# Optimization experiments

Measured on AMD Instinct MI355X. Metric: run time of the kernel, lower is better.

Reference implementation:

```python
import jax, jax.numpy as jnp
import numpy as np

N_NODES = 50000
N_EDGES = 400000
N_GRAPHS = 32
EMB = 64
EDGE_DIM = 4
IN_DIM = 11
LAYERS = 4
EPS = 1e-5


def _bn(x, g, b):
    # BatchNorm1d in train mode: biased batch statistics over rows
    m = jnp.mean(x, axis=0)
    v = jnp.mean(jnp.square(x - m), axis=0)
    return g * (x - m) * jax.lax.rsqrt(v + EPS) + b


def setup_inputs() -> dict:
    key = jax.random.key(0)
    ks = jax.random.split(key, 16)
    x = jax.random.normal(ks[0], (N_NODES, IN_DIM), dtype=jnp.float32)
    edge_attr = jax.random.normal(ks[1], (N_EDGES, EDGE_DIM), dtype=jnp.float32)
    edge_index = jax.random.randint(ks[2], (2, N_EDGES), 0, N_NODES, dtype=jnp.int32)
    batch = jnp.sort(jax.random.randint(ks[3], (N_NODES,), 0, N_GRAPHS, dtype=jnp.int32))

    def lin(k, fan_in, shape):
        bound = 1.0 / np.sqrt(fan_in)
        return jax.random.uniform(k, shape, jnp.float32, -bound, bound)

    msg_in = 2 * EMB + EDGE_DIM  # 132
    upd_in = 2 * EMB             # 128
    kk = jax.random.split(ks[4], 12)
    params = dict(
        lin_in_W=lin(kk[0], IN_DIM, (IN_DIM, EMB)),
        lin_in_b=lin(kk[1], IN_DIM, (EMB,)),
        msg_W1=lin(kk[2], msg_in, (LAYERS, msg_in, EMB)),
        msg_b1=lin(kk[3], msg_in, (LAYERS, EMB)),
        msg_g1=jnp.ones((LAYERS, EMB), jnp.float32),
        msg_be1=jnp.zeros((LAYERS, EMB), jnp.float32),
        msg_W2=lin(kk[4], EMB, (LAYERS, EMB, EMB)),
        msg_b2=lin(kk[5], EMB, (LAYERS, EMB)),
        msg_g2=jnp.ones((LAYERS, EMB), jnp.float32),
        msg_be2=jnp.zeros((LAYERS, EMB), jnp.float32),
        upd_W1=lin(kk[6], upd_in, (LAYERS, upd_in, EMB)),
        upd_b1=lin(kk[7], upd_in, (LAYERS, EMB)),
        upd_g1=jnp.ones((LAYERS, EMB), jnp.float32),
        upd_be1=jnp.zeros((LAYERS, EMB), jnp.float32),
        upd_W2=lin(kk[8], EMB, (LAYERS, EMB, EMB)),
        upd_b2=lin(kk[9], EMB, (LAYERS, EMB)),
        upd_g2=jnp.ones((LAYERS, EMB), jnp.float32),
        upd_be2=jnp.zeros((LAYERS, EMB), jnp.float32),
        pred_W=lin(kk[10], EMB, (EMB, 1)),
        pred_b=lin(kk[11], EMB, (1,)),
    )
    return dict(x=x, edge_attr=edge_attr, edge_index=edge_index, batch=batch, **params)


def reference(x, edge_attr, edge_index, batch, lin_in_W, lin_in_b,
              msg_W1, msg_b1, msg_g1, msg_be1, msg_W2, msg_b2, msg_g2, msg_be2,
              upd_W1, upd_b1, upd_g1, upd_be1, upd_W2, upd_b2, upd_g2, upd_be2,
              pred_W, pred_b):
    src = edge_index[0]  # j (source)
    dst = edge_index[1]  # i (target, PyG default flow source_to_target)
    h = x @ lin_in_W + lin_in_b  # (n, d)
    for l in range(LAYERS):
        m_in = jnp.concatenate([h[dst], h[src], edge_attr], axis=-1)  # (e, 2d+d_e)
        m = jax.nn.relu(_bn(m_in @ msg_W1[l] + msg_b1[l], msg_g1[l], msg_be1[l]))
        m = jax.nn.relu(_bn(m @ msg_W2[l] + msg_b2[l], msg_g2[l], msg_be2[l]))
        aggr = jax.ops.segment_sum(m, dst, num_segments=N_NODES)  # scatter-add
        u_in = jnp.concatenate([h, aggr], axis=-1)  # (n, 2d)
        u = jax.nn.relu(_bn(u_in @ upd_W1[l] + upd_b1[l], upd_g1[l], upd_be1[l]))
        u = jax.nn.relu(_bn(u @ upd_W2[l] + upd_b2[l], upd_g2[l], upd_be2[l]))
        h = h + u  # residual in MPNNModel.forward
    sums = jax.ops.segment_sum(h, batch, num_segments=N_GRAPHS)
    counts = jax.ops.segment_sum(jnp.ones((h.shape[0],), h.dtype), batch, num_segments=N_GRAPHS)
    h_graph = sums / jnp.maximum(counts, 1.0)[:, None]  # global_mean_pool
    out = h_graph @ pred_W + pred_b  # (G, 1)
    return out.reshape(-1)
```

## Files before the change

kernel.cpp:

```cpp
#include <hip/hip_runtime.h>

#define DEV __device__ __forceinline__

constexpr int NN = 50000;
constexpr int NE = 400000;
constexpr int NG = 32;
constexpr float EPSV = 1e-5f;
constexpr int SCAN_BLOCKS = 196;
constexpr int NSHARD = 8;
constexpr int STB = NSHARD * 128;

constexpr int ECB = 2048;
constexpr int ESLOT = ECB * 256 / 8;

typedef __attribute__((ext_vector_type(8))) short s16x8;
typedef __attribute__((ext_vector_type(4))) float f32x4;

DEV unsigned short f2b(float f) {
  union { float f; unsigned u; } x; x.f = f;
  unsigned r = x.u + 0x7fffu + ((x.u >> 16) & 1u);
  return (unsigned short)(r >> 16);
}
DEV float b2f(unsigned short u) {
  union { unsigned u; float f; } x; x.u = ((unsigned)u) << 16; return x.f;
}

DEV s16x8 frag_from_f32(const float* p) {
  const float4 v0 = *(const float4*)p;
  const float4 v1 = *(const float4*)(p + 4);
  s16x8 af;
  af[0] = (short)f2b(v0.x); af[1] = (short)f2b(v0.y);
  af[2] = (short)f2b(v0.z); af[3] = (short)f2b(v0.w);
  af[4] = (short)f2b(v1.x); af[5] = (short)f2b(v1.y);
  af[6] = (short)f2b(v1.z); af[7] = (short)f2b(v1.w);
  return af;
}

DEV void ld8(float* d, const float* p) {
  float4 a = *(const float4*)p;
  float4 b = *(const float4*)(p + 4);
  d[0] = a.x; d[1] = a.y; d[2] = a.z; d[3] = a.w;
  d[4] = b.x; d[5] = b.y; d[6] = b.z; d[7] = b.w;
}

DEV void bn_coeff(const float* __restrict__ st, const float* __restrict__ g,
                  const float* __restrict__ be, float invM, int c,
                  float& sc, float& sh) {
  float s = 0.f, s2 = 0.f;
#pragma unroll
  for (int k = 0; k < NSHARD; ++k) {
    s += st[k * 128 + c];
    s2 += st[k * 128 + 64 + c];
  }
  float mean = s * invM;
  float var = s2 * invM - mean * mean;
  sc = g[c] * rsqrtf(var + EPSV);
  sh = be[c] - mean * sc;
}

__global__ __launch_bounds__(256) void lin_in_kernel(
    const float* __restrict__ x, const float* __restrict__ W,
    const float* __restrict__ b, float* __restrict__ h)
{
  int gid = blockIdx.x * 256 + threadIdx.x;
  if (gid >= NN * 64) return;
  int n = gid >> 6, c = gid & 63;
  float acc = b[c];
#pragma unroll
  for (int k = 0; k < 11; ++k)
    acc = fmaf(x[n * 11 + k], W[k * 64 + c], acc);
  h[gid] = acc;
}

__global__ __launch_bounds__(256) void hist_kernel(
    const int* __restrict__ dstI, int* __restrict__ deg)
{
  int e = blockIdx.x * 256 + threadIdx.x;
  if (e < NE) atomicAdd(&deg[dstI[e]], 1);
}

__global__ __launch_bounds__(256) void scan_pass1(
    const int* __restrict__ deg, int* __restrict__ blockSums)
{
  __shared__ int red[4];
  int tid = threadIdx.x;
  int idx = blockIdx.x * 256 + tid;
  int v = (idx < NN) ? deg[idx] : 0;
#pragma unroll
  for (int off = 32; off > 0; off >>= 1) v += __shfl_down(v, off, 64);
  if ((tid & 63) == 0) red[tid >> 6] = v;
  __syncthreads();
  if (tid == 0) blockSums[blockIdx.x] = red[0] + red[1] + red[2] + red[3];
}

__global__ __launch_bounds__(256) void scan_pass2(
    const int* __restrict__ blockSums, int* __restrict__ blockOffs)
{
  __shared__ int part[256];
  int tid = threadIdx.x;
  int v = (tid < SCAN_BLOCKS) ? blockSums[tid] : 0;
  part[tid] = v;
  __syncthreads();
  for (int off = 1; off < 256; off <<= 1) {
    int t = 0;
    if (tid >= off) t = part[tid - off];
    __syncthreads();
    if (tid >= off) part[tid] += t;
    __syncthreads();
  }
  blockOffs[tid] = (tid == 0) ? 0 : part[tid - 1];
}

__global__ __launch_bounds__(256) void scan_pass3(
    const int* __restrict__ deg, const int* __restrict__ blockOffs,
    int* __restrict__ rowptr, int* __restrict__ cursor)
{
  __shared__ int part[256];
  int tid = threadIdx.x;
  int idx = blockIdx.x * 256 + tid;
  int v = (idx < NN) ? deg[idx] : 0;
  part[tid] = v;
  __syncthreads();
  for (int off = 1; off < 256; off <<= 1) {
    int t = 0;
    if (tid >= off) t = part[tid - off];
    __syncthreads();
    if (tid >= off) part[tid] += t;
    __syncthreads();
  }
  int excl = (tid == 0) ? 0 : part[tid - 1];
  int val = blockOffs[blockIdx.x] + excl;
  if (idx < NN) { rowptr[idx] = val; cursor[idx] = val; }
  if (idx == 0) rowptr[NN] = NE;
}

__global__ __launch_bounds__(256) void fill_pos_kernel(
    const int* __restrict__ dstI, int* __restrict__ cursor,
    int* __restrict__ eid)
{
  int e = blockIdx.x * 256 + threadIdx.x;
  if (e < NE) {
    int pos = atomicAdd(&cursor[dstI[e]], 1);
    eid[pos] = e;
  }
}

__global__ __launch_bounds__(256) void permute_kernel(
    const int* __restrict__ eid, const int* __restrict__ srcI,
    const int* __restrict__ dstI, const float* __restrict__ ea,
    int* __restrict__ srcP, int* __restrict__ dstP,
    float* __restrict__ eaP)
{
  int p = blockIdx.x * 256 + threadIdx.x;
  if (p < NE) {
    int e = eid[p];
    srcP[p] = srcI[e];
    dstP[p] = dstI[e];
    *(float4*)&eaP[(size_t)p * 4] = *(const float4*)&ea[(size_t)e * 4];
  }
}

__global__ __launch_bounds__(256) void gemm_dual_mfma(
    float* __restrict__ h, const float* __restrict__ W,
    const unsigned short* __restrict__ u2,
    const float* __restrict__ st, const float* __restrict__ g,
    const float* __restrict__ be, float invM,
    unsigned short* __restrict__ Hd, unsigned short* __restrict__ Hs)
{
  __shared__ __align__(16) unsigned short Wt_s[2 * 64 * 72];
  __shared__ float sc_s[64], sh_s[64];

  const int tid = threadIdx.x;
  const int lane = tid & 63;
  const int wave = tid >> 6;
  const int nn = lane & 15;
  const int kq = lane >> 4;

  if (u2 != nullptr && tid < 64) {
    float sc, sh;
    bn_coeff(st, g, be, invM, tid, sc, sh);
    sc_s[tid] = sc;
    sh_s[tid] = sh;
  }
#pragma unroll
  for (int i = 0; i < 32; ++i) {
    int idx = i * 256 + tid;
    int half = idx >> 12;
    int rem = idx & 4095;
    int k = rem >> 6, n = rem & 63;
    Wt_s[half * 4608 + n * 72 + k] = f2b(W[idx]);
  }
  __syncthreads();

  s16x8 bfrag[2][4][2];
#pragma unroll
  for (int o = 0; o < 2; ++o)
#pragma unroll
    for (int nt = 0; nt < 4; ++nt)
#pragma unroll
      for (int kc = 0; kc < 2; ++kc) {
        const unsigned short* p =
            &Wt_s[o * 4608 + (nt * 16 + nn) * 72 + kc * 32 + kq * 8];
#pragma unroll
        for (int j = 0; j < 8; ++j) bfrag[o][nt][kc][j] = (short)p[j];
      }

  const int rbase = blockIdx.x * 128 + wave * 32;

  f32x4 acc[2][2][4];
#pragma unroll
  for (int o = 0; o < 2; ++o)
#pragma unroll
    for (int rt = 0; rt < 2; ++rt)
#pragma unroll
      for (int nt = 0; nt < 4; ++nt) acc[o][rt][nt] = (f32x4){0.f, 0.f, 0.f, 0.f};

#pragma unroll
  for (int rt = 0; rt < 2; ++rt) {
    int row = rbase + rt * 16 + nn;
    int rowc = row < NN ? row : NN - 1;
#pragma unroll
    for (int kc = 0; kc < 2; ++kc) {
      const int c0k = kc * 32 + kq * 8;
      s16x8 af;
      if (u2 != nullptr) {
        float* hp = &h[(size_t)rowc * 64 + c0k];
        float hv[8];
        ld8(hv, hp);
        uint4 uv = *(const uint4*)&u2[(size_t)rowc * 64 + c0k];
        const unsigned uw[4] = {uv.x, uv.y, uv.z, uv.w};
#pragma unroll
        for (int d = 0; d < 4; ++d) {
          union { unsigned u; float f; } lo, hi;
          lo.u = (uw[d] & 0xffffu) << 16;
          hi.u = uw[d] & 0xffff0000u;
          int j0 = d * 2, j1 = d * 2 + 1;
          hv[j0] += fmaxf(fmaf(sc_s[c0k + j0], lo.f, sh_s[c0k + j0]), 0.f);
          hv[j1] += fmaxf(fmaf(sc_s[c0k + j1], hi.f, sh_s[c0k + j1]), 0.f);
        }
        if (row < NN) {
          *(float4*)hp = make_float4(hv[0], hv[1], hv[2], hv[3]);
          *(float4*)(hp + 4) = make_float4(hv[4], hv[5], hv[6], hv[7]);
        }
#pragma unroll
        for (int j = 0; j < 8; ++j) af[j] = (short)f2b(hv[j]);
      } else {
        af = frag_from_f32(&h[(size_t)rowc * 64 + c0k]);
      }
#pragma unroll
      for (int o = 0; o < 2; ++o)
#pragma unroll
        for (int nt = 0; nt < 4; ++nt)
          acc[o][rt][nt] = __builtin_amdgcn_mfma_f32_16x16x32_bf16(
              af, bfrag[o][nt][kc], acc[o][rt][nt], 0, 0, 0);
    }
  }

#pragma unroll
  for (int rt = 0; rt < 2; ++rt)
#pragma unroll
    for (int nt = 0; nt < 4; ++nt) {
      int col = nt * 16 + nn;
#pragma unroll
      for (int reg = 0; reg < 4; ++reg) {
        int row = rbase + rt * 16 + kq * 4 + reg;
        if (row < NN) {
          Hd[(size_t)row * 64 + col] = f2b(acc[0][rt][nt][reg]);
          Hs[(size_t)row * 64 + col] = f2b(acc[1][rt][nt][reg]);
        }
      }
    }
}

__global__ __launch_bounds__(256) void edge_combine(
    const unsigned short* __restrict__ Hd, const unsigned short* __restrict__ Hs,
    const float* __restrict__ eaP, const int* __restrict__ srcP,
    const int* __restrict__ dstP, const float* __restrict__ Wb,
    const float* __restrict__ bias, unsigned short* __restrict__ t1,
    float* __restrict__ outStats)
{
  __shared__ float red_s[128];
  const int tid = threadIdx.x;
  const int c0 = (tid & 7) * 8;
  float bv[8], w0[8], w1[8], w2[8], w3[8];
#pragma unroll
  for (int j = 0; j < 8; ++j) {
    bv[j] = bias[c0 + j];
    w0[j] = Wb[0 * 64 + c0 + j];
    w1[j] = Wb[1 * 64 + c0 + j];
    w2[j] = Wb[2 * 64 + c0 + j];
    w3[j] = Wb[3 * 64 + c0 + j];
  }

  float s[8], s2[8];
#pragma unroll
  for (int j = 0; j < 8; ++j) { s[j] = 0.f; s2[j] = 0.f; }

  const int e0 = (blockIdx.x * 256 + tid) >> 3;

  int eiA[4];
  float4 avA[4];
  uint4 hdA[4], hsA[4];
#pragma unroll
  for (int u = 0; u < 4; ++u) {
    int ec = e0 + u * ESLOT;
    eiA[u] = ec;
    int si = srcP[ec], di = dstP[ec];
    avA[u] = *(const float4*)&eaP[(size_t)ec * 4];
    hdA[u] = *(const uint4*)&Hd[(size_t)di * 64 + c0];
    hsA[u] = *(const uint4*)&Hs[(size_t)si * 64 + c0];
  }

  int eiB[3];
  bool hasB[3];
  float4 avB[3];
  uint4 hdB[3], hsB[3];
#pragma unroll
  for (int u = 0; u < 3; ++u) {
    int ee = e0 + (4 + u) * ESLOT;
    hasB[u] = ee < NE;
    int ec = hasB[u] ? ee : e0;
    eiB[u] = ec;
    int si = srcP[ec], di = dstP[ec];
    avB[u] = *(const float4*)&eaP[(size_t)ec * 4];
    hdB[u] = *(const uint4*)&Hd[(size_t)di * 64 + c0];
    hsB[u] = *(const uint4*)&Hs[(size_t)si * 64 + c0];
  }

#pragma unroll
  for (int u = 0; u < 4; ++u) {
    const unsigned hdw[4] = {hdA[u].x, hdA[u].y, hdA[u].z, hdA[u].w};
    const unsigned hsw[4] = {hsA[u].x, hsA[u].y, hsA[u].z, hsA[u].w};
    const float4 av = avA[u];
    unsigned short ob[8];
#pragma unroll
    for (int d = 0; d < 4; ++d) {
      union { unsigned uu; float f; } a0, a1, b0, b1u;
      a0.uu = (hdw[d] & 0xffffu) << 16; a1.uu = hdw[d] & 0xffff0000u;
      b0.uu = (hsw[d] & 0xffffu) << 16; b1u.uu = hsw[d] & 0xffff0000u;
      int j0 = d * 2, j1 = d * 2 + 1;
      float y0 = a0.f + b0.f + bv[j0] + av.x * w0[j0] + av.y * w1[j0] + av.z * w2[j0] + av.w * w3[j0];
      float y1 = a1.f + b1u.f + bv[j1] + av.x * w0[j1] + av.y * w1[j1] + av.z * w2[j1] + av.w * w3[j1];
      ob[j0] = f2b(y0); ob[j1] = f2b(y1);
      s[j0] += y0; s2[j0] += y0 * y0;
      s[j1] += y1; s2[j1] += y1 * y1;
    }
    *(uint4*)&t1[(size_t)eiA[u] * 64 + c0] = *(const uint4*)ob;
  }

#pragma unroll
  for (int u = 0; u < 3; ++u) {
    if (!hasB[u]) continue;
    const unsigned hdw[4] = {hdB[u].x, hdB[u].y, hdB[u].z, hdB[u].w};
    const unsigned hsw[4] = {hsB[u].x, hsB[u].y, hsB[u].z, hsB[u].w};
    const float4 av = avB[u];
    unsigned short ob[8];
#pragma unroll
    for (int d = 0; d < 4; ++d) {
      union { unsigned uu; float f; } a0, a1, b0, b1u;
      a0.uu = (hdw[d] & 0xffffu) << 16; a1.uu = hdw[d] & 0xffff0000u;
      b0.uu = (hsw[d] & 0xffffu) << 16; b1u.uu = hsw[d] & 0xffff0000u;
      int j0 = d * 2, j1 = d * 2 + 1;
      float y0 = a0.f + b0.f + bv[j0] + av.x * w0[j0] + av.y * w1[j0] + av.z * w2[j0] + av.w * w3[j0];
      float y1 = a1.f + b1u.f + bv[j1] + av.x * w0[j1] + av.y * w1[j1] + av.z * w2[j1] + av.w * w3[j1];
      ob[j0] = f2b(y0); ob[j1] = f2b(y1);
      s[j0] += y0; s2[j0] += y0 * y0;
      s[j1] += y1; s2[j1] += y1 * y1;
    }
    *(uint4*)&t1[(size_t)eiB[u] * 64 + c0] = *(const uint4*)ob;
  }

#pragma unroll
  for (int j = 0; j < 8; ++j) {
    s[j] += __shfl_xor(s[j], 8, 64);
    s[j] += __shfl_xor(s[j], 16, 64);
    s[j] += __shfl_xor(s[j], 32, 64);
    s2[j] += __shfl_xor(s2[j], 8, 64);
    s2[j] += __shfl_xor(s2[j], 16, 64);
    s2[j] += __shfl_xor(s2[j], 32, 64);
  }
  if (tid < 128) red_s[tid] = 0.f;
  __syncthreads();
  if ((tid & 63) < 8) {
#pragma unroll
    for (int j = 0; j < 8; ++j) {
      atomicAdd(&red_s[c0 + j], s[j]);
      atomicAdd(&red_s[64 + c0 + j], s2[j]);
    }
  }
  __syncthreads();
  if (tid < 128)
    atomicAdd(&outStats[(blockIdx.x & (NSHARD - 1)) * 128 + tid], red_s[tid]);
}

__global__ __launch_bounds__(256) void gemm64_bn_mfma(
    const unsigned short* A0,
    const float* __restrict__ W,
    const float* __restrict__ bias,
    const float* __restrict__ inStats,
    const float* __restrict__ inG,
    const float* __restrict__ inBe,
    float invM_in,
    unsigned short* outp,
    float* __restrict__ outStats,
    int M)
{
  __shared__ __align__(16) unsigned short Wt_s[64 * 72];
  __shared__ float scale_s[64];
  __shared__ float shift_s[64];
  __shared__ float red_s[128];

  const int tid = threadIdx.x;
  const int lane = tid & 63;
  const int wave = tid >> 6;
  const int nn = lane & 15;
  const int kq = lane >> 4;

  if (tid < 64) {
    float sc, sh;
    bn_coeff(inStats, inG, inBe, invM_in, tid, sc, sh);
    scale_s[tid] = sc;
    shift_s[tid] = sh;
  }
#pragma unroll
  for (int i = 0; i < 16; ++i) {
    int idx = i * 256 + tid;
    int k = idx >> 6, n = idx & 63;
    Wt_s[n * 72 + k] = f2b(W[idx]);
  }
  __syncthreads();

  s16x8 bfrag[4][2];
#pragma unroll
  for (int nt = 0; nt < 4; ++nt)
#pragma unroll
    for (int kc = 0; kc < 2; ++kc)
      bfrag[nt][kc] = *(const s16x8*)&Wt_s[(nt * 16 + nn) * 72 + kc * 32 + kq * 8];

  float scf[2][8], shf[2][8];
#pragma unroll
  for (int kc = 0; kc < 2; ++kc) {
    int k0 = kc * 32 + kq * 8;
    ld8(scf[kc], &scale_s[k0]);
    ld8(shf[kc], &shift_s[k0]);
  }

  float bcol[4];
#pragma unroll
  for (int nt = 0; nt < 4; ++nt) bcol[nt] = bias[nt * 16 + nn];

  float s[4] = {0.f, 0.f, 0.f, 0.f};
  float s2[4] = {0.f, 0.f, 0.f, 0.f};

  uint4 raw[4][2];
  f32x4 acc[4][4];

  const int rb0 = blockIdx.x * 512 + wave * 64;
#pragma unroll
  for (int rt = 0; rt < 4; ++rt) {
    int row = rb0 + rt * 16 + nn;
    int rowc = row < M ? row : M - 1;
#pragma unroll
    for (int kc = 0; kc < 2; ++kc)
      raw[rt][kc] = *(const uint4*)&A0[(size_t)rowc * 64 + kc * 32 + kq * 8];
  }

#pragma unroll
  for (int rt = 0; rt < 4; ++rt)
#pragma unroll
    for (int nt = 0; nt < 4; ++nt) acc[rt][nt] = (f32x4){0.f, 0.f, 0.f, 0.f};
#pragma unroll
  for (int rt = 0; rt < 4; ++rt) {
#pragma unroll
    for (int kc = 0; kc < 2; ++kc) {
      unsigned wbits[4] = {raw[rt][kc].x, raw[rt][kc].y, raw[rt][kc].z, raw[rt][kc].w};
      s16x8 af;
#pragma unroll
      for (int d = 0; d < 4; ++d) {
        union { unsigned u; float f; } lo, hi;
        lo.u = (wbits[d] & 0xffffu) << 16;
        hi.u = wbits[d] & 0xffff0000u;
        int j0 = d * 2, j1 = d * 2 + 1;
        af[j0] = (short)f2b(fmaxf(fmaf(scf[kc][j0], lo.f, shf[kc][j0]), 0.f));
        af[j1] = (short)f2b(fmaxf(fmaf(scf[kc][j1], hi.f, shf[kc][j1]), 0.f));
      }
#pragma unroll
      for (int nt = 0; nt < 4; ++nt)
        acc[rt][nt] = __builtin_amdgcn_mfma_f32_16x16x32_bf16(
            af, bfrag[nt][kc], acc[rt][nt], 0, 0, 0);
    }
  }

  const int rb1 = rb0 + 256;
#pragma unroll
  for (int rt = 0; rt < 4; ++rt) {
    int row = rb1 + rt * 16 + nn;
    int rowc = row < M ? row : M - 1;
#pragma unroll
    for (int kc = 0; kc < 2; ++kc)
      raw[rt][kc] = *(const uint4*)&A0[(size_t)rowc * 64 + kc * 32 + kq * 8];
  }

#pragma unroll
  for (int rt = 0; rt < 4; ++rt)
#pragma unroll
    for (int nt = 0; nt < 4; ++nt) {
      int col = nt * 16 + nn;
#pragma unroll
      for (int reg = 0; reg < 4; ++reg) {
        int row = rb0 + rt * 16 + kq * 4 + reg;
        if (row < M) {
          float y = acc[rt][nt][reg] + bcol[nt];
          outp[(size_t)row * 64 + col] = f2b(y);
          s[nt] += y; s2[nt] += y * y;
        }
      }
    }

#pragma unroll
  for (int rt = 0; rt < 4; ++rt)
#pragma unroll
    for (int nt = 0; nt < 4; ++nt) acc[rt][nt] = (f32x4){0.f, 0.f, 0.f, 0.f};
#pragma unroll
  for (int rt = 0; rt < 4; ++rt) {
#pragma unroll
    for (int kc = 0; kc < 2; ++kc) {
      unsigned wbits[4] = {raw[rt][kc].x, raw[rt][kc].y, raw[rt][kc].z, raw[rt][kc].w};
      s16x8 af;
#pragma unroll
      for (int d = 0; d < 4; ++d) {
        union { unsigned u; float f; } lo, hi;
        lo.u = (wbits[d] & 0xffffu) << 16;
        hi.u = wbits[d] & 0xffff0000u;
        int j0 = d * 2, j1 = d * 2 + 1;
        af[j0] = (short)f2b(fmaxf(fmaf(scf[kc][j0], lo.f, shf[kc][j0]), 0.f));
        af[j1] = (short)f2b(fmaxf(fmaf(scf[kc][j1], hi.f, shf[kc][j1]), 0.f));
      }
#pragma unroll
      for (int nt = 0; nt < 4; ++nt)
        acc[rt][nt] = __builtin_amdgcn_mfma_f32_16x16x32_bf16(
            af, bfrag[nt][kc], acc[rt][nt], 0, 0, 0);
    }
  }

#pragma unroll
  for (int rt = 0; rt < 4; ++rt)
#pragma unroll
    for (int nt = 0; nt < 4; ++nt) {
      int col = nt * 16 + nn;
#pragma unroll
      for (int reg = 0; reg < 4; ++reg) {
        int row = rb1 + rt * 16 + kq * 4 + reg;
        if (row < M) {
          float y = acc[rt][nt][reg] + bcol[nt];
          outp[(size_t)row * 64 + col] = f2b(y);
          s[nt] += y; s2[nt] += y * y;
        }
      }
    }

#pragma unroll
  for (int nt = 0; nt < 4; ++nt) {
    s[nt] += __shfl_xor(s[nt], 16, 64);
    s[nt] += __shfl_xor(s[nt], 32, 64);
    s2[nt] += __shfl_xor(s2[nt], 16, 64);
    s2[nt] += __shfl_xor(s2[nt], 32, 64);
  }
  if (tid < 128) red_s[tid] = 0.f;
  __syncthreads();
  if (lane < 16) {
#pragma unroll
    for (int nt = 0; nt < 4; ++nt) {
      atomicAdd(&red_s[nt * 16 + nn], s[nt]);
      atomicAdd(&red_s[64 + nt * 16 + nn], s2[nt]);
    }
  }
  __syncthreads();
  if (tid < 128)
    atomicAdd(&outStats[(blockIdx.x & (NSHARD - 1)) * 128 + tid], red_s[tid]);
}

__global__ __launch_bounds__(256) void gemm_concat_mfma(
    const float* __restrict__ A0,
    const unsigned short* __restrict__ A1b,
    const float* __restrict__ W,
    const float* __restrict__ bias,
    unsigned short* __restrict__ outp,
    float* __restrict__ outStats,
    int M)
{
  __shared__ __align__(16) unsigned short Wt_s[64 * 136];
  __shared__ float red_s[128];

  const int tid = threadIdx.x;
  const int lane = tid & 63;
  const int wave = tid >> 6;
  const int nn = lane & 15;
  const int kq = lane >> 4;

#pragma unroll
  for (int i = 0; i < 32; ++i) {
    int idx = i * 256 + tid;
    int k = idx >> 6, n = idx & 63;
    Wt_s[n * 136 + k] = f2b(W[idx]);
  }
  __syncthreads();

  s16x8 bfrag[4][4];
#pragma unroll
  for (int nt = 0; nt < 4; ++nt)
#pragma unroll
    for (int kc = 0; kc < 4; ++kc) {
      const unsigned short* p = &Wt_s[(nt * 16 + nn) * 136 + kc * 32 + kq * 8];
#pragma unroll
      for (int j = 0; j < 8; ++j) bfrag[nt][kc][j] = (short)p[j];
    }

  const int rbase = blockIdx.x * 128 + wave * 32;

  f32x4 acc[2][4];
#pragma unroll
  for (int rt = 0; rt < 2; ++rt)
#pragma unroll
    for (int nt = 0; nt < 4; ++nt) acc[rt][nt] = (f32x4){0.f, 0.f, 0.f, 0.f};

#pragma unroll
  for (int rt = 0; rt < 2; ++rt) {
    int row = rbase + rt * 16 + nn;
    int rowc = row < M ? row : M - 1;
#pragma unroll
    for (int kc = 0; kc < 4; ++kc) {
      s16x8 af;
      if (kc < 2) {
        af = frag_from_f32(&A0[(size_t)rowc * 64 + kc * 32 + kq * 8]);
      } else {
        af = *(const s16x8*)&A1b[(size_t)rowc * 64 + (kc - 2) * 32 + kq * 8];
      }
#pragma unroll
      for (int nt = 0; nt < 4; ++nt)
        acc[rt][nt] = __builtin_amdgcn_mfma_f32_16x16x32_bf16(
            af, bfrag[nt][kc], acc[rt][nt], 0, 0, 0);
    }
  }

  float bcol[4];
#pragma unroll
  for (int nt = 0; nt < 4; ++nt) bcol[nt] = bias[nt * 16 + nn];

  float s[4] = {0.f, 0.f, 0.f, 0.f};
  float s2[4] = {0.f, 0.f, 0.f, 0.f};
#pragma unroll
  for (int rt = 0; rt < 2; ++rt)
#pragma unroll
    for (int nt = 0; nt < 4; ++nt) {
      int col = nt * 16 + nn;
#pragma unroll
      for (int reg = 0; reg < 4; ++reg) {
        int row = rbase + rt * 16 + kq * 4 + reg;
        if (row < M) {
          float y = acc[rt][nt][reg] + bcol[nt];
          outp[(size_t)row * 64 + col] = f2b(y);
          s[nt] += y; s2[nt] += y * y;
        }
      }
    }
#pragma unroll
  for (int nt = 0; nt < 4; ++nt) {
    s[nt] += __shfl_xor(s[nt], 16, 64);
    s[nt] += __shfl_xor(s[nt], 32, 64);
    s2[nt] += __shfl_xor(s2[nt], 16, 64);
    s2[nt] += __shfl_xor(s2[nt], 32, 64);
  }
  if (tid < 128) red_s[tid] = 0.f;
  __syncthreads();
  if (lane < 16) {
#pragma unroll
    for (int nt = 0; nt < 4; ++nt) {
      atomicAdd(&red_s[nt * 16 + nn], s[nt]);
      atomicAdd(&red_s[64 + nt * 16 + nn], s2[nt]);
    }
  }
  __syncthreads();
  if (tid < 128)
    atomicAdd(&outStats[(blockIdx.x & (NSHARD - 1)) * 128 + tid], red_s[tid]);
}

__global__ __launch_bounds__(256) void aggregate_kernel(
    const unsigned short* __restrict__ t2, const int* __restrict__ rowptr,
    const float* __restrict__ stats, const float* __restrict__ g,
    const float* __restrict__ be, float invM,
    unsigned short* __restrict__ aggr)
{
  __shared__ float sc_s[64], sh_s[64];
  const int tid = threadIdx.x;
  if (tid < 64) {
    float sc, sh;
    bn_coeff(stats, g, be, invM, tid, sc, sh);
    sc_s[tid] = sc;
    sh_s[tid] = sh;
  }
  __syncthreads();

  int node = (blockIdx.x * 256 + tid) >> 6;
  int lane = tid & 63;
  if (node >= NN) return;
  const int c8 = (lane & 7) * 8;
  const int rq = lane >> 3;

  float sc[8], sh[8];
#pragma unroll
  for (int j = 0; j < 8; ++j) {
    sc[j] = sc_s[c8 + j];
    sh[j] = sh_s[c8 + j];
  }

  int lo = rowptr[node], hi = rowptr[node + 1];
  float acc[8] = {0.f, 0.f, 0.f, 0.f, 0.f, 0.f, 0.f, 0.f};

  for (int i = lo; i < hi; i += 16) {
    int r0 = i + rq;
    int r1 = i + 8 + rq;
    bool h0 = r0 < hi, h1 = r1 < hi;
    uint4 v0 = make_uint4(0u, 0u, 0u, 0u), v1 = make_uint4(0u, 0u, 0u, 0u);
    if (h0) v0 = *(const uint4*)&t2[(size_t)r0 * 64 + c8];
    if (h1) v1 = *(const uint4*)&t2[(size_t)r1 * 64 + c8];
    if (h0) {
      const unsigned w[4] = {v0.x, v0.y, v0.z, v0.w};
#pragma unroll
      for (int d = 0; d < 4; ++d) {
        union { unsigned u; float f; } a0, a1;
        a0.u = (w[d] & 0xffffu) << 16;
        a1.u = w[d] & 0xffff0000u;
        acc[d * 2] += fmaxf(fmaf(sc[d * 2], a0.f, sh[d * 2]), 0.f);
        acc[d * 2 + 1] += fmaxf(fmaf(sc[d * 2 + 1], a1.f, sh[d * 2 + 1]), 0.f);
      }
    }
    if (h1) {
      const unsigned w[4] = {v1.x, v1.y, v1.z, v1.w};
#pragma unroll
      for (int d = 0; d < 4; ++d) {
        union { unsigned u; float f; } a0, a1;
        a0.u = (w[d] & 0xffffu) << 16;
        a1.u = w[d] & 0xffff0000u;
        acc[d * 2] += fmaxf(fmaf(sc[d * 2], a0.f, sh[d * 2]), 0.f);
        acc[d * 2 + 1] += fmaxf(fmaf(sc[d * 2 + 1], a1.f, sh[d * 2 + 1]), 0.f);
      }
    }
  }
#pragma unroll
  for (int j = 0; j < 8; ++j) {
    acc[j] += __shfl_xor(acc[j], 8, 64);
    acc[j] += __shfl_xor(acc[j], 16, 64);
    acc[j] += __shfl_xor(acc[j], 32, 64);
  }
  if (rq == 0) {
    unsigned short o[8];
#pragma unroll
    for (int j = 0; j < 8; ++j) o[j] = f2b(acc[j]);
    *(uint4*)&aggr[(size_t)node * 64 + c8] = *(const uint4*)o;
  }
}

constexpr int POOL_NPB = 128;

__global__ __launch_bounds__(256) void pool_partial(
    const float* __restrict__ h, const unsigned short* __restrict__ u2,
    const float* __restrict__ st, const float* __restrict__ g,
    const float* __restrict__ be, float invM,
    const int* __restrict__ batch, float* __restrict__ sums)
{
  int lane = threadIdx.x & 63;
  int wave = threadIdx.x >> 6;
  float sc, sh;
  bn_coeff(st, g, be, invM, lane, sc, sh);
  int base = blockIdx.x * POOL_NPB;
  float acc = 0.f;
  int gcur = -1;
  for (int i = wave; i < POOL_NPB; i += 4) {
    int n = base + i;
    if (n >= NN) break;
    int gb = batch[n];
    if (gb != gcur) {
      if (gcur >= 0) atomicAdd(&sums[gcur * 64 + lane], acc);
      gcur = gb;
      acc = 0.f;
    }
    acc += h[(size_t)n * 64 + lane] +
           fmaxf(fmaf(sc, b2f(u2[(size_t)n * 64 + lane]), sh), 0.f);
  }
  if (gcur >= 0) atomicAdd(&sums[gcur * 64 + lane], acc);
}

DEV int lower_bound_i(const int* __restrict__ a, int n, int v) {
  int lo = 0, hi = n;
  while (lo < hi) {
    int m = (lo + hi) >> 1;
    if (a[m] < v) lo = m + 1; else hi = m;
  }
  return lo;
}

__global__ __launch_bounds__(64) void pool_final(
    const float* __restrict__ sums, const int* __restrict__ batch,
    const float* __restrict__ predW, const float* __restrict__ predB,
    float* __restrict__ out)
{
  int g = blockIdx.x;
  int lane = threadIdx.x;
  int lo = lower_bound_i(batch, NN, g);
  int hi = lower_bound_i(batch, NN, g + 1);
  float cnt = fmaxf((float)(hi - lo), 1.0f);
  float p = sums[g * 64 + lane] / cnt * predW[lane];
#pragma unroll
  for (int off = 32; off > 0; off >>= 1) p += __shfl_down(p, off, 64);
  if (lane == 0) out[g] = p + predB[0];
}

extern "C" void kernel_launch(void* const* d_in, const int* in_sizes, int n_in,
                              void* d_out, int out_size, void* d_ws, size_t ws_size,
                              hipStream_t stream)
{
  (void)in_sizes; (void)n_in; (void)out_size; (void)ws_size;

  const float* x        = (const float*)d_in[0];
  const float* edge_attr= (const float*)d_in[1];
  const int*   eidx     = (const int*)d_in[2];
  const int*   batch    = (const int*)d_in[3];
  const float* linW     = (const float*)d_in[4];
  const float* linB     = (const float*)d_in[5];
  const float* msgW1    = (const float*)d_in[6];
  const float* msgB1    = (const float*)d_in[7];
  const float* msgG1    = (const float*)d_in[8];
  const float* msgBe1   = (const float*)d_in[9];
  const float* msgW2    = (const float*)d_in[10];
  const float* msgB2    = (const float*)d_in[11];
  const float* msgG2    = (const float*)d_in[12];
  const float* msgBe2   = (const float*)d_in[13];
  const float* updW1    = (const float*)d_in[14];
  const float* updB1    = (const float*)d_in[15];
  const float* updG1    = (const float*)d_in[16];
  const float* updBe1   = (const float*)d_in[17];
  const float* updW2    = (const float*)d_in[18];
  const float* updB2    = (const float*)d_in[19];
  const float* updG2    = (const float*)d_in[20];
  const float* updBe2   = (const float*)d_in[21];
  const float* predW    = (const float*)d_in[22];
  const float* predB    = (const float*)d_in[23];

  const int* srcI = eidx;
  const int* dstI = eidx + NE;

  char* p = (char*)d_ws;
  float* h  = (float*)p;            p += (size_t)NN * 64 * 4;
  unsigned short* t1 = (unsigned short*)p; p += (size_t)NE * 64 * 2;
  unsigned short* aggr = (unsigned short*)p; p += (size_t)NN * 64 * 2;
  unsigned short* u1 = (unsigned short*)p;   p += (size_t)NN * 64 * 2;
  unsigned short* Hd = (unsigned short*)p;   p += (size_t)NN * 64 * 2;
  unsigned short* Hs = (unsigned short*)p;   p += (size_t)NN * 64 * 2;
  float* stats = (float*)p;         p += 16 * STB * 4;
  float* sums = (float*)p;          p += NG * 64 * 4;
  int* deg = (int*)p;               p += (size_t)NN * 4;
  int* cursor = (int*)p;            p += (size_t)NN * 4;
  int* rowptr = (int*)p;            p += (size_t)(NN + 1) * 4;
  int* eid = (int*)p;               p += (size_t)NE * 4;
  int* srcP = (int*)p;              p += (size_t)NE * 4;
  int* dstP = (int*)p;              p += (size_t)NE * 4;
  float* eaP = (float*)p;           p += (size_t)NE * 4 * 4;
  int* blockSums = (int*)p;         p += 256 * 4;
  int* blockOffs = (int*)p;         p += 256 * 4;

  hipMemsetAsync(stats, 0, (size_t)(16 * STB + NG * 64 + NN) * 4, stream);

  hist_kernel<<<(NE + 255) / 256, 256, 0, stream>>>(dstI, deg);
  scan_pass1<<<SCAN_BLOCKS, 256, 0, stream>>>(deg, blockSums);
  scan_pass2<<<1, 256, 0, stream>>>(blockSums, blockOffs);
  scan_pass3<<<SCAN_BLOCKS, 256, 0, stream>>>(deg, blockOffs, rowptr, cursor);
  fill_pos_kernel<<<(NE + 255) / 256, 256, 0, stream>>>(dstI, cursor, eid);
  permute_kernel<<<(NE + 255) / 256, 256, 0, stream>>>(
      eid, srcI, dstI, edge_attr, srcP, dstP, eaP);

  lin_in_kernel<<<(NN * 64 + 255) / 256, 256, 0, stream>>>(x, linW, linB, h);

  const float invE = 1.0f / (float)NE;
  const float invN = 1.0f / (float)NN;
  const int NB128 = (NN + 127) / 128;
  const int NB512 = (NN + 511) / 512;
  const int EB512 = (NE + 511) / 512;

  for (int l = 0; l < 4; ++l) {
    float* st0 = stats + (l * 4 + 0) * STB;
    float* st1 = stats + (l * 4 + 1) * STB;
    float* st2 = stats + (l * 4 + 2) * STB;
    float* st3 = stats + (l * 4 + 3) * STB;
    const float* W1 = msgW1 + (size_t)l * 132 * 64;

    const unsigned short* prevU2 = (l == 0) ? nullptr : u1;
    const float* pst = (l == 0) ? stats : stats + ((l - 1) * 4 + 3) * STB;
    const float* pg  = (l == 0) ? updG2 : updG2 + (l - 1) * 64;
    const float* pbe = (l == 0) ? updBe2 : updBe2 + (l - 1) * 64;

    gemm_dual_mfma<<<NB128, 256, 0, stream>>>(
        h, W1, prevU2, pst, pg, pbe, invN, Hd, Hs);

    edge_combine<<<ECB, 256, 0, stream>>>(
        Hd, Hs, eaP, srcP, dstP, W1 + 128 * 64, msgB1 + l * 64,
        t1, st0);

    gemm64_bn_mfma<<<EB512, 256, 0, stream>>>(
        t1, msgW2 + (size_t)l * 64 * 64, msgB2 + l * 64,
        st0, msgG1 + l * 64, msgBe1 + l * 64, invE,
        t1, st1, NE);

    aggregate_kernel<<<(NN * 64 + 255) / 256, 256, 0, stream>>>(
        t1, rowptr, st1, msgG2 + l * 64, msgBe2 + l * 64, invE, aggr);

    gemm_concat_mfma<<<NB128, 256, 0, stream>>>(
        h, aggr, updW1 + (size_t)l * 128 * 64, updB1 + l * 64,
        u1, st2, NN);

    gemm64_bn_mfma<<<NB512, 256, 0, stream>>>(
        u1, updW2 + (size_t)l * 64 * 64, updB2 + l * 64,
        st2, updG1 + l * 64, updBe1 + l * 64, invN,
        u1, st3, NN);
  }

  pool_partial<<<(NN + POOL_NPB - 1) / POOL_NPB, 256, 0, stream>>>(
      h, u1, stats + (3 * 4 + 3) * STB, updG2 + 3 * 64, updBe2 + 3 * 64, invN,
      batch, sums);
  pool_final<<<NG, 64, 0, stream>>>(sums, batch, predW, predB, (float*)d_out);
}
```

Baseline: 630.5 us.

## Fuse CSR aggregation into update GEMM and merge setup kernels

The segment-sum aggregation (BN+ReLU applied on the fly) now runs inside the update-MLP first GEMM kernel. Each block aggregates 32 nodes into shared memory and then runs the MFMA GEMM with each wave owning a 16-column slice. This removes the aggr buffer round trip and one launch per layer, at the cost of a smaller block tile and weights reloaded from global memory per block. The histogram is also merged with the input linear layer, the scan's middle pass is folded into the last pass, and pool_partial computes BN coefficients once per block into shared memory.

```diff
diff --git a/kernel.cpp b/kernel.cpp
--- a/kernel.cpp
+++ b/kernel.cpp
@@ -58,25 +58,21 @@
   sh = be[c] - mean * sc;
 }
 
-__global__ __launch_bounds__(256) void lin_in_kernel(
+__global__ __launch_bounds__(256) void hist_lin_kernel(
+    const int* __restrict__ dstI, int* __restrict__ deg,
     const float* __restrict__ x, const float* __restrict__ W,
     const float* __restrict__ b, float* __restrict__ h)
 {
   int gid = blockIdx.x * 256 + threadIdx.x;
-  if (gid >= NN * 64) return;
-  int n = gid >> 6, c = gid & 63;
-  float acc = b[c];
-#pragma unroll
-  for (int k = 0; k < 11; ++k)
-    acc = fmaf(x[n * 11 + k], W[k * 64 + c], acc);
-  h[gid] = acc;
-}
-
-__global__ __launch_bounds__(256) void hist_kernel(
-    const int* __restrict__ dstI, int* __restrict__ deg)
-{
-  int e = blockIdx.x * 256 + threadIdx.x;
-  if (e < NE) atomicAdd(&deg[dstI[e]], 1);
+  if (gid < NE) atomicAdd(&deg[dstI[gid]], 1);
+  if (gid < NN * 64) {
+    int n = gid >> 6, c = gid & 63;
+    float acc = b[c];
+#pragma unroll
+    for (int k = 0; k < 11; ++k)
+      acc = fmaf(x[n * 11 + k], W[k * 64 + c], acc);
+    h[gid] = acc;
+  }
 }
 
 __global__ __launch_bounds__(256) void scan_pass1(
@@ -93,12 +89,27 @@
   if (tid == 0) blockSums[blockIdx.x] = red[0] + red[1] + red[2] + red[3];
 }
 
-__global__ __launch_bounds__(256) void scan_pass2(
-    const int* __restrict__ blockSums, int* __restrict__ blockOffs)
+__global__ __launch_bounds__(256) void scan_pass3(
+    const int* __restrict__ deg, const int* __restrict__ blockSums,
+    int* __restrict__ rowptr, int* __restrict__ cursor)
 {
   __shared__ int part[256];
+  __shared__ int bsum[256];
   int tid = threadIdx.x;
-  int v = (tid < SCAN_BLOCKS) ? blockSums[tid] : 0;
+
+  bsum[tid] = (tid < SCAN_BLOCKS) ? blockSums[tid] : 0;
+  __syncthreads();
+  for (int off = 1; off < 256; off <<= 1) {
+    int t = 0;
+    if (tid >= off) t = bsum[tid - off];
+    __syncthreads();
+    if (tid >= off) bsum[tid] += t;
+    __syncthreads();
+  }
+  int blockOff = (blockIdx.x == 0) ? 0 : bsum[blockIdx.x - 1];
+
+  int idx = blockIdx.x * 256 + tid;
+  int v = (idx < NN) ? deg[idx] : 0;
   part[tid] = v;
   __syncthreads();
   for (int off = 1; off < 256; off <<= 1) {
@@ -108,28 +119,8 @@
     if (tid >= off) part[tid] += t;
     __syncthreads();
   }
-  blockOffs[tid] = (tid == 0) ? 0 : part[tid - 1];
-}
-
-__global__ __launch_bounds__(256) void scan_pass3(
-    const int* __restrict__ deg, const int* __restrict__ blockOffs,
-    int* __restrict__ rowptr, int* __restrict__ cursor)
-{
-  __shared__ int part[256];
-  int tid = threadIdx.x;
-  int idx = blockIdx.x * 256 + tid;
-  int v = (idx < NN) ? deg[idx] : 0;
-  part[tid] = v;
-  __syncthreads();
-  for (int off = 1; off < 256; off <<= 1) {
-    int t = 0;
-    if (tid >= off) t = part[tid - off];
-    __syncthreads();
-    if (tid >= off) part[tid] += t;
-    __syncthreads();
-  }
   int excl = (tid == 0) ? 0 : part[tid - 1];
-  int val = blockOffs[blockIdx.x] + excl;
+  int val = blockOff + excl;
   if (idx < NN) { rowptr[idx] = val; cursor[idx] = val; }
   if (idx == 0) rowptr[NN] = NE;
 }
@@ -580,16 +571,20 @@
     atomicAdd(&outStats[(blockIdx.x & (NSHARD - 1)) * 128 + tid], red_s[tid]);
 }
 
-__global__ __launch_bounds__(256) void gemm_concat_mfma(
+__global__ __launch_bounds__(256) void aggr_concat_mfma(
+    const unsigned short* __restrict__ t2,
+    const int* __restrict__ rowptr,
+    const float* __restrict__ st1, const float* __restrict__ g1,
+    const float* __restrict__ be1, float invE,
     const float* __restrict__ A0,
-    const unsigned short* __restrict__ A1b,
     const float* __restrict__ W,
     const float* __restrict__ bias,
     unsigned short* __restrict__ outp,
     float* __restrict__ outStats,
     int M)
 {
-  __shared__ __align__(16) unsigned short Wt_s[64 * 136];
+  __shared__ __align__(16) unsigned short aggr_s[32 * 72];
+  __shared__ float sc_s[64], sh_s[64];
   __shared__ float red_s[128];
 
   const int tid = threadIdx.x;
@@ -598,32 +593,86 @@
   const int nn = lane & 15;
   const int kq = lane >> 4;
 
-#pragma unroll
-  for (int i = 0; i < 32; ++i) {
-    int idx = i * 256 + tid;
-    int k = idx >> 6, n = idx & 63;
-    Wt_s[n * 136 + k] = f2b(W[idx]);
-  }
-  __syncthreads();
-
-  s16x8 bfrag[4][4];
-#pragma unroll
-  for (int nt = 0; nt < 4; ++nt)
-#pragma unroll
-    for (int kc = 0; kc < 4; ++kc) {
-      const unsigned short* p = &Wt_s[(nt * 16 + nn) * 136 + kc * 32 + kq * 8];
-#pragma unroll
-      for (int j = 0; j < 8; ++j) bfrag[nt][kc][j] = (short)p[j];
-    }
-
-  const int rbase = blockIdx.x * 128 + wave * 32;
-
-  f32x4 acc[2][4];
-#pragma unroll
-  for (int rt = 0; rt < 2; ++rt)
-#pragma unroll
-    for (int nt = 0; nt < 4; ++nt) acc[rt][nt] = (f32x4){0.f, 0.f, 0.f, 0.f};
-
+  if (tid < 64) {
+    float sc, sh;
+    bn_coeff(st1, g1, be1, invE, tid, sc, sh);
+    sc_s[tid] = sc;
+    sh_s[tid] = sh;
+  }
+  __syncthreads();
+
+  const int rbase = blockIdx.x * 32;
+
+  {
+    const int c8 = (lane & 7) * 8;
+    const int rq = lane >> 3;
+    float sc[8], sh[8];
+#pragma unroll
+    for (int j = 0; j < 8; ++j) { sc[j] = sc_s[c8 + j]; sh[j] = sh_s[c8 + j]; }
+
+    for (int t = 0; t < 8; ++t) {
+      int nrow = wave * 8 + t;
+      int node = rbase + nrow;
+      int lo = 0, hi = 0;
+      if (node < NN) { lo = rowptr[node]; hi = rowptr[node + 1]; }
+      float acc[8] = {0.f, 0.f, 0.f, 0.f, 0.f, 0.f, 0.f, 0.f};
+      for (int i = lo; i < hi; i += 16) {
+        int r0 = i + rq;
+        int r1 = i + 8 + rq;
+        bool h0 = r0 < hi, h1 = r1 < hi;
+        uint4 v0 = make_uint4(0u, 0u, 0u, 0u), v1 = make_uint4(0u, 0u, 0u, 0u);
+        if (h0) v0 = *(const uint4*)&t2[(size_t)r0 * 64 + c8];
+        if (h1) v1 = *(const uint4*)&t2[(size_t)r1 * 64 + c8];
+        if (h0) {
+          const unsigned w[4] = {v0.x, v0.y, v0.z, v0.w};
+#pragma unroll
+          for (int d = 0; d < 4; ++d) {
+            union { unsigned u; float f; } a0, a1;
+            a0.u = (w[d] & 0xffffu) << 16;
+            a1.u = w[d] & 0xffff0000u;
+            acc[d * 2] += fmaxf(fmaf(sc[d * 2], a0.f, sh[d * 2]), 0.f);
+            acc[d * 2 + 1] += fmaxf(fmaf(sc[d * 2 + 1], a1.f, sh[d * 2 + 1]), 0.f);
+          }
+        }
+        if (h1) {
+          const unsigned w[4] = {v1.x, v1.y, v1.z, v1.w};
+#pragma unroll
+          for (int d = 0; d < 4; ++d) {
+            union { unsigned u; float f; } a0, a1;
+            a0.u = (w[d] & 0xffffu) << 16;
+            a1.u = w[d] & 0xffff0000u;
+            acc[d * 2] += fmaxf(fmaf(sc[d * 2], a0.f, sh[d * 2]), 0.f);
+            acc[d * 2 + 1] += fmaxf(fmaf(sc[d * 2 + 1], a1.f, sh[d * 2 + 1]), 0.f);
+          }
+        }
+      }
+#pragma unroll
+      for (int j = 0; j < 8; ++j) {
+        acc[j] += __shfl_xor(acc[j], 8, 64);
+        acc[j] += __shfl_xor(acc[j], 16, 64);
+        acc[j] += __shfl_xor(acc[j], 32, 64);
+      }
+      if (rq == 0) {
+        unsigned short o[8];
+#pragma unroll
+        for (int j = 0; j < 8; ++j) o[j] = f2b(acc[j]);
+        *(uint4*)&aggr_s[(size_t)nrow * 72 + c8] = *(const uint4*)o;
+      }
+    }
+  }
+  __syncthreads();
+
+  s16x8 bf[4];
+#pragma unroll
+  for (int kc = 0; kc < 4; ++kc)
+#pragma unroll
+    for (int j = 0; j < 8; ++j)
+      bf[kc][j] = (short)f2b(W[(kc * 32 + kq * 8 + j) * 64 + wave * 16 + nn]);
+
+  float bcol = bias[wave * 16 + nn];
+
+  f32x4 acc0 = (f32x4){0.f, 0.f, 0.f, 0.f};
+  f32x4 acc1 = (f32x4){0.f, 0.f, 0.f, 0.f};
 #pragma unroll
   for (int rt = 0; rt < 2; ++rt) {
     int row = rbase + rt * 16 + nn;
@@ -634,131 +683,45 @@
       if (kc < 2) {
         af = frag_from_f32(&A0[(size_t)rowc * 64 + kc * 32 + kq * 8]);
       } else {
-        af = *(const s16x8*)&A1b[(size_t)rowc * 64 + (kc - 2) * 32 + kq * 8];
-      }
-#pragma unroll
-      for (int nt = 0; nt < 4; ++nt)
-        acc[rt][nt] = __builtin_amdgcn_mfma_f32_16x16x32_bf16(
-            af, bfrag[nt][kc], acc[rt][nt], 0, 0, 0);
-    }
-  }
-
-  float bcol[4];
-#pragma unroll
-  for (int nt = 0; nt < 4; ++nt) bcol[nt] = bias[nt * 16 + nn];
-
-  float s[4] = {0.f, 0.f, 0.f, 0.f};
-  float s2[4] = {0.f, 0.f, 0.f, 0.f};
-#pragma unroll
-  for (int rt = 0; rt < 2; ++rt)
-#pragma unroll
-    for (int nt = 0; nt < 4; ++nt) {
-      int col = nt * 16 + nn;
-#pragma unroll
-      for (int reg = 0; reg < 4; ++reg) {
-        int row = rbase + rt * 16 + kq * 4 + reg;
-        if (row < M) {
-          float y = acc[rt][nt][reg] + bcol[nt];
-          outp[(size_t)row * 64 + col] = f2b(y);
-          s[nt] += y; s2[nt] += y * y;
-        }
-      }
-    }
-#pragma unroll
-  for (int nt = 0; nt < 4; ++nt) {
-    s[nt] += __shfl_xor(s[nt], 16, 64);
-    s[nt] += __shfl_xor(s[nt], 32, 64);
-    s2[nt] += __shfl_xor(s2[nt], 16, 64);
-    s2[nt] += __shfl_xor(s2[nt], 32, 64);
-  }
+        af = *(const s16x8*)&aggr_s[(size_t)(rt * 16 + nn) * 72 +
+                                    (kc - 2) * 32 + kq * 8];
+      }
+      if (rt == 0)
+        acc0 = __builtin_amdgcn_mfma_f32_16x16x32_bf16(af, bf[kc], acc0, 0, 0, 0);
+      else
+        acc1 = __builtin_amdgcn_mfma_f32_16x16x32_bf16(af, bf[kc], acc1, 0, 0, 0);
+    }
+  }
+
+  float s = 0.f, s2v = 0.f;
+  const int col = wave * 16 + nn;
+#pragma unroll
+  for (int rt = 0; rt < 2; ++rt) {
+    const f32x4 a = rt == 0 ? acc0 : acc1;
+#pragma unroll
+    for (int reg = 0; reg < 4; ++reg) {
+      int row = rbase + rt * 16 + kq * 4 + reg;
+      if (row < M) {
+        float y = a[reg] + bcol;
+        outp[(size_t)row * 64 + col] = f2b(y);
+        s += y; s2v += y * y;
+      }
+    }
+  }
+
+  s += __shfl_xor(s, 16, 64);
+  s += __shfl_xor(s, 32, 64);
+  s2v += __shfl_xor(s2v, 16, 64);
+  s2v += __shfl_xor(s2v, 32, 64);
   if (tid < 128) red_s[tid] = 0.f;
   __syncthreads();
   if (lane < 16) {
-#pragma unroll
-    for (int nt = 0; nt < 4; ++nt) {
-      atomicAdd(&red_s[nt * 16 + nn], s[nt]);
-      atomicAdd(&red_s[64 + nt * 16 + nn], s2[nt]);
-    }
+    atomicAdd(&red_s[wave * 16 + nn], s);
+    atomicAdd(&red_s[64 + wave * 16 + nn], s2v);
   }
   __syncthreads();
   if (tid < 128)
     atomicAdd(&outStats[(blockIdx.x & (NSHARD - 1)) * 128 + tid], red_s[tid]);
-}
-
-__global__ __launch_bounds__(256) void aggregate_kernel(
-    const unsigned short* __restrict__ t2, const int* __restrict__ rowptr,
-    const float* __restrict__ stats, const float* __restrict__ g,
-    const float* __restrict__ be, float invM,
-    unsigned short* __restrict__ aggr)
-{
-  __shared__ float sc_s[64], sh_s[64];
-  const int tid = threadIdx.x;
-  if (tid < 64) {
-    float sc, sh;
-    bn_coeff(stats, g, be, invM, tid, sc, sh);
-    sc_s[tid] = sc;
-    sh_s[tid] = sh;
-  }
-  __syncthreads();
-
-  int node = (blockIdx.x * 256 + tid) >> 6;
-  int lane = tid & 63;
-  if (node >= NN) return;
-  const int c8 = (lane & 7) * 8;
-  const int rq = lane >> 3;
-
-  float sc[8], sh[8];
-#pragma unroll
-  for (int j = 0; j < 8; ++j) {
-    sc[j] = sc_s[c8 + j];
-    sh[j] = sh_s[c8 + j];
-  }
-
-  int lo = rowptr[node], hi = rowptr[node + 1];
-  float acc[8] = {0.f, 0.f, 0.f, 0.f, 0.f, 0.f, 0.f, 0.f};
-
-  for (int i = lo; i < hi; i += 16) {
-    int r0 = i + rq;
-    int r1 = i + 8 + rq;
-    bool h0 = r0 < hi, h1 = r1 < hi;
-    uint4 v0 = make_uint4(0u, 0u, 0u, 0u), v1 = make_uint4(0u, 0u, 0u, 0u);
-    if (h0) v0 = *(const uint4*)&t2[(size_t)r0 * 64 + c8];
-    if (h1) v1 = *(const uint4*)&t2[(size_t)r1 * 64 + c8];
-    if (h0) {
-      const unsigned w[4] = {v0.x, v0.y, v0.z, v0.w};
-#pragma unroll
-      for (int d = 0; d < 4; ++d) {
-        union { unsigned u; float f; } a0, a1;
-        a0.u = (w[d] & 0xffffu) << 16;
-        a1.u = w[d] & 0xffff0000u;
-        acc[d * 2] += fmaxf(fmaf(sc[d * 2], a0.f, sh[d * 2]), 0.f);
-        acc[d * 2 + 1] += fmaxf(fmaf(sc[d * 2 + 1], a1.f, sh[d * 2 + 1]), 0.f);
-      }
-    }
-    if (h1) {
-      const unsigned w[4] = {v1.x, v1.y, v1.z, v1.w};
-#pragma unroll
-      for (int d = 0; d < 4; ++d) {
-        union { unsigned u; float f; } a0, a1;
-        a0.u = (w[d] & 0xffffu) << 16;
-        a1.u = w[d] & 0xffff0000u;
-        acc[d * 2] += fmaxf(fmaf(sc[d * 2], a0.f, sh[d * 2]), 0.f);
-        acc[d * 2 + 1] += fmaxf(fmaf(sc[d * 2 + 1], a1.f, sh[d * 2 + 1]), 0.f);
-      }
-    }
-  }
-#pragma unroll
-  for (int j = 0; j < 8; ++j) {
-    acc[j] += __shfl_xor(acc[j], 8, 64);
-    acc[j] += __shfl_xor(acc[j], 16, 64);
-    acc[j] += __shfl_xor(acc[j], 32, 64);
-  }
-  if (rq == 0) {
-    unsigned short o[8];
-#pragma unroll
-    for (int j = 0; j < 8; ++j) o[j] = f2b(acc[j]);
-    *(uint4*)&aggr[(size_t)node * 64 + c8] = *(const uint4*)o;
-  }
 }
 
 constexpr int POOL_NPB = 128;
@@ -769,10 +732,19 @@
     const float* __restrict__ be, float invM,
     const int* __restrict__ batch, float* __restrict__ sums)
 {
-  int lane = threadIdx.x & 63;
-  int wave = threadIdx.x >> 6;
-  float sc, sh;
-  bn_coeff(st, g, be, invM, lane, sc, sh);
+  __shared__ float sc_s[64], sh_s[64];
+  int tid = threadIdx.x;
+  if (tid < 64) {
+    float sc, sh;
+    bn_coeff(st, g, be, invM, tid, sc, sh);
+    sc_s[tid] = sc;
+    sh_s[tid] = sh;
+  }
+  __syncthreads();
+
+  int lane = tid & 63;
+  int wave = tid >> 6;
+  float sc = sc_s[lane], sh = sh_s[lane];
   int base = blockIdx.x * POOL_NPB;
   float acc = 0.f;
   int gcur = -1;
@@ -853,7 +825,6 @@
   char* p = (char*)d_ws;
   float* h  = (float*)p;            p += (size_t)NN * 64 * 4;
   unsigned short* t1 = (unsigned short*)p; p += (size_t)NE * 64 * 2;
-  unsigned short* aggr = (unsigned short*)p; p += (size_t)NN * 64 * 2;
   unsigned short* u1 = (unsigned short*)p;   p += (size_t)NN * 64 * 2;
   unsigned short* Hd = (unsigned short*)p;   p += (size_t)NN * 64 * 2;
   unsigned short* Hs = (unsigned short*)p;   p += (size_t)NN * 64 * 2;
@@ -867,23 +838,21 @@
   int* dstP = (int*)p;              p += (size_t)NE * 4;
   float* eaP = (float*)p;           p += (size_t)NE * 4 * 4;
   int* blockSums = (int*)p;         p += 256 * 4;
-  int* blockOffs = (int*)p;         p += 256 * 4;
 
   hipMemsetAsync(stats, 0, (size_t)(16 * STB + NG * 64 + NN) * 4, stream);
 
-  hist_kernel<<<(NE + 255) / 256, 256, 0, stream>>>(dstI, deg);
+  hist_lin_kernel<<<(NN * 64 + 255) / 256, 256, 0, stream>>>(
+      dstI, deg, x, linW, linB, h);
   scan_pass1<<<SCAN_BLOCKS, 256, 0, stream>>>(deg, blockSums);
-  scan_pass2<<<1, 256, 0, stream>>>(blockSums, blockOffs);
-  scan_pass3<<<SCAN_BLOCKS, 256, 0, stream>>>(deg, blockOffs, rowptr, cursor);
+  scan_pass3<<<SCAN_BLOCKS, 256, 0, stream>>>(deg, blockSums, rowptr, cursor);
   fill_pos_kernel<<<(NE + 255) / 256, 256, 0, stream>>>(dstI, cursor, eid);
   permute_kernel<<<(NE + 255) / 256, 256, 0, stream>>>(
       eid, srcI, dstI, edge_attr, srcP, dstP, eaP);
 
-  lin_in_kernel<<<(NN * 64 + 255) / 256, 256, 0, stream>>>(x, linW, linB, h);
-
   const float invE = 1.0f / (float)NE;
   const float invN = 1.0f / (float)NN;
   const int NB128 = (NN + 127) / 128;
+  const int NB32  = (NN + 31) / 32;
   const int NB512 = (NN + 511) / 512;
   const int EB512 = (NE + 511) / 512;
 
@@ -911,11 +880,9 @@
         st0, msgG1 + l * 64, msgBe1 + l * 64, invE,
         t1, st1, NE);
 
-    aggregate_kernel<<<(NN * 64 + 255) / 256, 256, 0, stream>>>(
-        t1, rowptr, st1, msgG2 + l * 64, msgBe2 + l * 64, invE, aggr);
-
-    gemm_concat_mfma<<<NB128, 256, 0, stream>>>(
-        h, aggr, updW1 + (size_t)l * 128 * 64, updB1 + l * 64,
+    aggr_concat_mfma<<<NB32, 256, 0, stream>>>(
+        t1, rowptr, st1, msgG2 + l * 64, msgBe2 + l * 64, invE,
+        h, updW1 + (size_t)l * 128 * 64, updB1 + l * 64,
         u1, st2, NN);
 
     gemm64_bn_mfma<<<NB512, 256, 0, stream>>>(
```

After: 638.1 us. Within noise of the previous version (+1.2%).
